# Kernel tuning notes

Measured on AMD Instinct MI355X. Metric: run time of the kernel, lower is better.

The kernel has to match this reference:

```python
import jax, jax.numpy as jnp
import numpy as np

DIM = 768
NUM_HEADS = 12
DIM_HEAD = 64
INNER = NUM_HEADS * DIM_HEAD  # 768
SCALE = DIM_HEAD ** -0.5


def setup_inputs() -> dict:
    key = jax.random.key(0)
    k1, k2, k3 = jax.random.split(key, 3)
    B, N = 8, 1024
    x = jax.random.normal(k1, (B, N, DIM), dtype=jnp.float32)
    # Linear(dim, 3*inner_dim, bias=False): weight shape (out, in) torch-style
    w_qkv = jax.random.normal(k2, (3 * INNER, DIM), dtype=jnp.float32) * (DIM ** -0.5)
    # proj: Linear(inner_dim, dim, bias=False)
    w_proj = jax.random.normal(k3, (DIM, INNER), dtype=jnp.float32) * (INNER ** -0.5)
    return {"x": x, "w_qkv": w_qkv, "w_proj": w_proj}


def reference(x, w_qkv, w_proj):
    B, N, C = x.shape
    H, dh = NUM_HEADS, DIM_HEAD
    # qkv projection: (B,N,C) @ (C, 3*inner) -> (B,N,3*inner)
    qkv = jnp.einsum('bnc,oc->bno', x, w_qkv)
    qkv = qkv.reshape(B, N, 3, H, dh).transpose(2, 0, 3, 1, 4)  # (3,B,H,N,dh)
    q, k, v = qkv[0], qkv[1], qkv[2]
    # attention scores (B,H,N,N)
    attn_scores = jnp.einsum('bhnd,bhmd->bhnm', q, k) * SCALE
    attn_probs = jax.nn.softmax(attn_scores, axis=-1)
    # attention output (B,H,N,dh) -> (B,N,inner)
    attn_out = jnp.einsum('bhnm,bhmd->bhnd', attn_probs, v)
    attn_out = attn_out.transpose(0, 2, 1, 3).reshape(B, N, H * dh)
    out = jnp.einsum('bni,oi->bno', attn_out, w_proj)
    return out
```

## Files before the change

kernel.cpp:

```cpp
#include <hip/hip_runtime.h>
#include <stdint.h>

typedef unsigned short u16;
typedef __attribute__((ext_vector_type(8))) short short8;
typedef __attribute__((ext_vector_type(4))) short short4v;
typedef __attribute__((ext_vector_type(4))) float f32x4;

#define LOG2E 1.44269504088896340736f

#define Bb 8
#define NSEQ 1024
#define DIMC 768
#define NH 12
#define DH 64
#define INNER 768
#define MTOT (Bb*NSEQ)
#define QKVN (3*INNER)
#define HEADS_TOT (Bb*NH)
#define QKV_PART ((size_t)Bb*NH*NSEQ*DH)

static __device__ inline u16 f2bf(float f) {
    uint32_t u = __builtin_bit_cast(uint32_t, f);
    uint32_t r = (u + 0x7fffu + ((u >> 16) & 1u)) >> 16;
    return (u16)r;
}

static __device__ __forceinline__ uint32_t pkbf(float f0, float f1) {
    uint32_t u0 = __builtin_bit_cast(uint32_t, f0) + 0x8000u;
    uint32_t u1 = __builtin_bit_cast(uint32_t, f1) + 0x8000u;
    return __builtin_amdgcn_perm(u1, u0, 0x07060302u);
}

#if __has_builtin(__builtin_amdgcn_mfma_f32_16x16x16bf16_1k)
static __device__ __forceinline__ f32x4 mfma16(short4v a, short4v b, f32x4 c) {
    return __builtin_amdgcn_mfma_f32_16x16x16bf16_1k(a, b, c, 0, 0, 0);
}
#else
static __device__ __forceinline__ f32x4 mfma16(short4v a, short4v b, f32x4 c) {
    asm volatile("v_mfma_f32_16x16x16_bf16 %0, %1, %2, %0\n\ts_nop 7\n\ts_nop 7"
                 : "+v"(c) : "v"(a), "v"(b));
    return c;
}
#endif

typedef __attribute__((address_space(1))) const void gas_void;
typedef __attribute__((address_space(3))) void las_void;
static __device__ __forceinline__ void async16(u16* lds, const u16* g) {
    __builtin_amdgcn_global_load_lds((gas_void*)(uintptr_t)g,
                                     (las_void*)(uintptr_t)lds, 16, 0, 0);
}

static __device__ __forceinline__ void wait_vm0() {
    __builtin_amdgcn_s_waitcnt(0x0f70);
}

#define NX8  786432
#define NWQ8 221184
#define NWP8 73728
#define NCVT (NX8 + NWQ8 + NWP8)
__global__ __launch_bounds__(256) void cvt_all(const float* __restrict__ x,
                                               const float* __restrict__ wq,
                                               const float* __restrict__ wp,
                                               u16* __restrict__ xb,
                                               u16* __restrict__ wqb,
                                               u16* __restrict__ wpb) {
    int i = blockIdx.x * 256 + threadIdx.x;
    const float* s; u16* d; int j;
    if (i < NX8) { s = x; d = xb; j = i; }
    else if (i < NX8 + NWQ8) { s = wq; d = wqb; j = i - NX8; }
    else { s = wp; d = wpb; j = i - NX8 - NWQ8; }
    const float4* s4 = (const float4*)s;
    float4 a = s4[2 * j], b = s4[2 * j + 1];
    float v[8] = {a.x, a.y, a.z, a.w, b.x, b.y, b.z, b.w};
    u16 o[8];
#pragma unroll
    for (int t = 0; t < 8; t++) o[t] = f2bf(v[t]);
    ((uint4*)d)[j] = *(const uint4*)o;
}

#define BK 32
__global__ __launch_bounds__(512, 4) void gemm_qkv(const u16* __restrict__ A,
                                                   const u16* __restrict__ Bm,
                                                   u16* __restrict__ qkv) {
    __shared__ u16 As[2][128 * BK];
    __shared__ u16 Bs[2][256 * BK];
    const int tid = threadIdx.x;
    const int w = tid >> 6, lane = tid & 63, quad = lane >> 4, l16 = lane & 15;
    const int wr = w >> 2, wc = w & 3;
    const int bid = blockIdx.x + 9 * blockIdx.y;
    const int xcd = bid & 7, j9 = bid >> 3;
    const int m0 = (8 * xcd + j9 / 9) * 128;
    const int n0 = (j9 % 9) * 256;
    const int K = DIMC;

    const int rl = lane >> 2, cc = lane & 3;
    const int ra = w * 16 + rl;
    const u16* agp = A + (size_t)(m0 + ra) * K + ((cc - ((ra >> 1) & 3)) & 3) * 8;
    const int aslot = (w * 16) * BK;
    const u16* bgp[2]; int bslot[2];
#pragma unroll
    for (int j = 0; j < 2; j++) {
        int rb = w * 32 + j * 16 + rl;
        bgp[j] = Bm + (size_t)(n0 + rb) * K + ((cc - ((rb >> 1) & 3)) & 3) * 8;
        bslot[j] = (w * 32 + j * 16) * BK;
    }

    const int swz = ((quad + ((l16 >> 1) & 3)) & 3) * 8;
    int aoff[4], boff[4];
#pragma unroll
    for (int t = 0; t < 4; t++) {
        aoff[t] = (wr * 64 + t * 16 + l16) * BK + swz;
        boff[t] = (wc * 64 + t * 16 + l16) * BK + swz;
    }

    async16(&As[0][aslot], agp);
    async16(&Bs[0][bslot[0]], bgp[0]);
    async16(&Bs[0][bslot[1]], bgp[1]);

    f32x4 acc[4][4] = {};
    const int NIT = K / BK;
    for (int it = 0; it < NIT; ++it) {
        const int cur = it & 1, nxt = cur ^ 1;
        wait_vm0();
        __syncthreads();
        if (it + 1 < NIT) {
            int ktn = (it + 1) * BK;
            async16(&As[nxt][aslot], agp + ktn);
            async16(&Bs[nxt][bslot[0]], bgp[0] + ktn);
            async16(&Bs[nxt][bslot[1]], bgp[1] + ktn);
        }
        short8 af[4], bf[4];
#pragma unroll
        for (int t = 0; t < 4; t++) af[t] = *(const short8*)(&As[cur][aoff[t]]);
#pragma unroll
        for (int t = 0; t < 4; t++) bf[t] = *(const short8*)(&Bs[cur][boff[t]]);
#pragma unroll
        for (int mt = 0; mt < 4; mt++)
#pragma unroll
            for (int nt = 0; nt < 4; nt++)
                acc[mt][nt] = __builtin_amdgcn_mfma_f32_16x16x32_bf16(af[mt], bf[nt],
                                                                      acc[mt][nt], 0, 0, 0);
    }

#pragma unroll
    for (int nt = 0; nt < 4; nt++) {
        int o = n0 + wc * 64 + nt * 16 + l16;
        int which = o / 768;
        int rem = o - which * 768;
        int h = rem >> 6, d = rem & 63;
        if (which == 2) {
            u16* vt = qkv + 2 * QKV_PART;
#pragma unroll
            for (int mt = 0; mt < 4; mt++) {
                int m = m0 + wr * 64 + mt * 16 + quad * 4;
                int bb = m >> 10, ns = m & 1023;
                alignas(8) u16 pk[4];
#pragma unroll
                for (int r = 0; r < 4; r++) pk[r] = f2bf(acc[mt][nt][r]);
                *(uint2*)(vt + ((size_t)(bb * NH + h) * DH + d) * NSEQ + ns) =
                    *(const uint2*)pk;
            }
        } else {
            float sc = (which == 0) ? (0.125f * LOG2E) : 1.0f;
#pragma unroll
            for (int mt = 0; mt < 4; mt++)
#pragma unroll
                for (int r = 0; r < 4; r++) {
                    int m = m0 + wr * 64 + mt * 16 + quad * 4 + r;
                    int bb = m >> 10, ns = m & 1023;
                    size_t idx = (size_t)which * QKV_PART +
                                 (((size_t)(bb * NH + h) * NSEQ + ns) << 6) + d;
                    qkv[idx] = f2bf(acc[mt][nt][r] * sc);
                }
        }
    }
}

__global__ __launch_bounds__(256) void gemm_proj(const u16* __restrict__ A,
                                                 const u16* __restrict__ Bm,
                                                 float* __restrict__ Co) {
    __shared__ u16 As[2][128 * BK];
    __shared__ u16 Bs[2][128 * BK];
    const int tid = threadIdx.x;
    const int w = tid >> 6, lane = tid & 63, quad = lane >> 4, l16 = lane & 15;
    const int wr = w >> 1, wc = w & 1;
    const int m0 = blockIdx.y * 128;
    const int n0 = blockIdx.x * 128;
    const int K = INNER, N = DIMC;

    const int rl = lane >> 2, cc = lane & 3;
    const u16* ag[2]; const u16* bg[2]; int sl[2];
#pragma unroll
    for (int j = 0; j < 2; j++) {
        int r = w * 32 + j * 16 + rl;
        int c = ((cc - ((r >> 1) & 3)) & 3) * 8;
        ag[j] = A + (size_t)(m0 + r) * K + c;
        bg[j] = Bm + (size_t)(n0 + r) * K + c;
        sl[j] = (w * 32 + j * 16) * BK;
    }
    const int swz = ((quad + ((l16 >> 1) & 3)) & 3) * 8;
    int aoff[4], boff[4];
#pragma unroll
    for (int t = 0; t < 4; t++) {
        aoff[t] = (wr * 64 + t * 16 + l16) * BK + swz;
        boff[t] = (wc * 64 + t * 16 + l16) * BK + swz;
    }

#pragma unroll
    for (int j = 0; j < 2; j++) {
        async16(&As[0][sl[j]], ag[j]);
        async16(&Bs[0][sl[j]], bg[j]);
    }

    f32x4 acc[4][4] = {};
    const int NIT = K / BK;
    for (int it = 0; it < NIT; ++it) {
        const int cur = it & 1, nxt = cur ^ 1;
        wait_vm0();
        __syncthreads();
        if (it + 1 < NIT) {
            int ktn = (it + 1) * BK;
#pragma unroll
            for (int j = 0; j < 2; j++) {
                async16(&As[nxt][sl[j]], ag[j] + ktn);
                async16(&Bs[nxt][sl[j]], bg[j] + ktn);
            }
        }
        short8 af[4], bf[4];
#pragma unroll
        for (int t = 0; t < 4; t++) af[t] = *(const short8*)(&As[cur][aoff[t]]);
#pragma unroll
        for (int t = 0; t < 4; t++) bf[t] = *(const short8*)(&Bs[cur][boff[t]]);
#pragma unroll
        for (int mt = 0; mt < 4; mt++)
#pragma unroll
            for (int nt = 0; nt < 4; nt++)
                acc[mt][nt] = __builtin_amdgcn_mfma_f32_16x16x32_bf16(af[mt], bf[nt],
                                                                      acc[mt][nt], 0, 0, 0);
    }
#pragma unroll
    for (int mt = 0; mt < 4; mt++)
#pragma unroll
        for (int nt = 0; nt < 4; nt++) {
            int o = n0 + wc * 64 + nt * 16 + l16;
#pragma unroll
            for (int r = 0; r < 4; r++) {
                int m = m0 + wr * 64 + mt * 16 + quad * 4 + r;
                Co[(size_t)m * N + o] = acc[mt][nt][r];
            }
        }
}

__global__ __launch_bounds__(256) void attn_kernel(const u16* __restrict__ qkv,
                                                   u16* __restrict__ attn) {
    __shared__ u16 Ks[2][64 * 64];
    __shared__ u16 Vs[2][64 * 64];

    const int tid = threadIdx.x;
    const int w = tid >> 6, lane = tid & 63, quad = lane >> 4, l16 = lane & 15;
    const int bh = blockIdx.x, qt = blockIdx.y;
    const size_t headoff = (size_t)bh * NSEQ * DH;
    const u16* Qp = qkv + headoff;
    const u16* Kp = qkv + QKV_PART + headoff;
    const u16* Vtp = qkv + 2 * QKV_PART + headoff;
    const int q0 = qt * 128 + w * 32;

    const int rl8 = lane >> 3, cc8 = lane & 7;
    const u16* kg[2]; const u16* vg[2]; int ksl[2];
#pragma unroll
    for (int j = 0; j < 2; j++) {
        int r = w * 16 + j * 8 + rl8;
        int c = ((cc8 - r) & 7) * 8;
        kg[j] = Kp + (size_t)r * DH + c;
        vg[j] = Vtp + (size_t)r * NSEQ + c;
        ksl[j] = (w * 16 + j * 8) * 64;
    }

    const int sw0 = ((quad + l16) & 7) * 8;
    const int sw1 = ((quad + 4 + l16) & 7) * 8;

    short8 qf[2][2];
#pragma unroll
    for (int mf = 0; mf < 2; mf++) {
        qf[mf][0] = *(const short8*)(Qp + (size_t)(q0 + mf * 16 + l16) * DH + quad * 8);
        qf[mf][1] = *(const short8*)(Qp + (size_t)(q0 + mf * 16 + l16) * DH + 32 + quad * 8);
    }

#pragma unroll
    for (int j = 0; j < 2; j++) {
        async16(&Ks[0][ksl[j]], kg[j]);
        async16(&Vs[0][ksl[j]], vg[j]);
    }

    f32x4 oacc[2][4] = {};
    float lsum[2] = {0.f, 0.f};

    const int NIT = NSEQ / 64;
    for (int it = 0; it < NIT; ++it) {
        const int cur = it & 1, nxt = cur ^ 1;
        wait_vm0();
        __syncthreads();
        if (it + 1 < NIT) {
            int ktn = (it + 1) * 64;
#pragma unroll
            for (int j = 0; j < 2; j++) {
                async16(&Ks[nxt][ksl[j]], kg[j] + (size_t)ktn * DH);
                async16(&Vs[nxt][ksl[j]], vg[j] + ktn);
            }
        }

        short8 kf[4][2];
#pragma unroll
        for (int nt = 0; nt < 4; nt++) {
            const u16* kr = &Ks[cur][(nt * 16 + l16) * 64];
            kf[nt][0] = *(const short8*)(kr + sw0);
            kf[nt][1] = *(const short8*)(kr + sw1);
        }
        short4v vf[4][4];
#pragma unroll
        for (int nt2 = 0; nt2 < 4; nt2++) {
            int row = nt2 * 16 + l16;
#pragma unroll
            for (int c = 0; c < 4; c++) {
                int off = row * 64 + (((c * 2 + (quad >> 1) + row) & 7) << 3) + (quad & 1) * 4;
                vf[nt2][c] = *(const short4v*)(&Vs[cur][off]);
            }
        }

#pragma unroll
        for (int mf = 0; mf < 2; mf++) {
            f32x4 st[4];
#pragma unroll
            for (int nt = 0; nt < 4; nt++) {
                f32x4 z = {};
                z = __builtin_amdgcn_mfma_f32_16x16x32_bf16(kf[nt][0], qf[mf][0], z, 0, 0, 0);
                z = __builtin_amdgcn_mfma_f32_16x16x32_bf16(kf[nt][1], qf[mf][1], z, 0, 0, 0);
                st[nt] = z;
            }
            short4v pf[4];
#pragma unroll
            for (int c = 0; c < 4; c++) {
                float p0 = __builtin_amdgcn_exp2f(st[c][0]);
                float p1 = __builtin_amdgcn_exp2f(st[c][1]);
                float p2 = __builtin_amdgcn_exp2f(st[c][2]);
                float p3 = __builtin_amdgcn_exp2f(st[c][3]);
                lsum[mf] += (p0 + p1) + (p2 + p3);
                uint2 u = {pkbf(p0, p1), pkbf(p2, p3)};
                pf[c] = __builtin_bit_cast(short4v, u);
            }
#pragma unroll
            for (int nt2 = 0; nt2 < 4; nt2++)
#pragma unroll
                for (int c = 0; c < 4; c++)
                    oacc[mf][nt2] = mfma16(vf[nt2][c], pf[c], oacc[mf][nt2]);
        }
    }

#pragma unroll
    for (int mf = 0; mf < 2; mf++) {
        float v = lsum[mf];
        v += __shfl_xor(v, 16);
        v += __shfl_xor(v, 32);
        lsum[mf] = 1.0f / v;
    }

    const int b = bh / NH, h = bh - (bh / NH) * NH;
#pragma unroll
    for (int mf = 0; mf < 2; mf++) {
        int q = q0 + mf * 16 + l16;
        float inv = lsum[mf];
#pragma unroll
        for (int nt2 = 0; nt2 < 4; nt2++) {
            uint2 u = {pkbf(oacc[mf][nt2][0] * inv, oacc[mf][nt2][1] * inv),
                       pkbf(oacc[mf][nt2][2] * inv, oacc[mf][nt2][3] * inv)};
            int d = nt2 * 16 + quad * 4;
            *(uint2*)(attn + ((size_t)(b * NSEQ + q)) * INNER + h * DH + d) = u;
        }
    }
}

extern "C" void kernel_launch(void* const* d_in, const int* in_sizes, int n_in,
                              void* d_out, int out_size, void* d_ws, size_t ws_size,
                              hipStream_t stream) {
    const float* x = (const float*)d_in[0];
    const float* w_qkv = (const float*)d_in[1];
    const float* w_proj = (const float*)d_in[2];
    float* out = (float*)d_out;

    u16* xb = (u16*)d_ws;
    u16* wqkvb = xb + 6291456;
    u16* wprojb = wqkvb + 1769472;
    u16* qkvb = wprojb + 589824;
    u16* attnb = qkvb + 18874368;

    cvt_all<<<NCVT / 256, 256, 0, stream>>>(x, w_qkv, w_proj, xb, wqkvb, wprojb);

    dim3 g1(QKVN / 256, MTOT / 128);
    gemm_qkv<<<g1, 512, 0, stream>>>(xb, wqkvb, qkvb);

    dim3 g2(HEADS_TOT, NSEQ / 128);
    attn_kernel<<<g2, 256, 0, stream>>>(qkvb, attnb);

    dim3 g3(INNER / 128, MTOT / 128);
    gemm_proj<<<g3, 256, 0, stream>>>(attnb, wprojb, out);
}
```

Baseline: 186.5 us.

## Triple-buffer LDS with counted vmcnt waits and shrink proj GEMM tile

Converts the QKV GEMM, attention and projection GEMM loops from double to triple LDS buffering with a prefetch distance of two. Each loop now waits on a partial vmcnt instead of draining all loads, so the newest stage can stay in flight while the current one is computed, and it uses a bare s_barrier. The projection GEMM tile shrinks from 128x128 to 64x128, giving more blocks to fill the CUs. The cost is more LDS per block, which may limit occupancy, and waitcnt counts that must exactly match the number of loads issued per stage.

```diff
diff --git a/kernel.cpp b/kernel.cpp
--- a/kernel.cpp
+++ b/kernel.cpp
@@ -50,8 +50,9 @@
                                      (las_void*)(uintptr_t)lds, 16, 0, 0);
 }
 
-static __device__ __forceinline__ void wait_vm0() {
-    __builtin_amdgcn_s_waitcnt(0x0f70);
+template <int N>
+static __device__ __forceinline__ void wait_vm() {
+    __builtin_amdgcn_s_waitcnt(0x0f70 | N);
 }
 
 #define NX8  786432
@@ -82,8 +83,8 @@
 __global__ __launch_bounds__(512, 4) void gemm_qkv(const u16* __restrict__ A,
                                                    const u16* __restrict__ Bm,
                                                    u16* __restrict__ qkv) {
-    __shared__ u16 As[2][128 * BK];
-    __shared__ u16 Bs[2][256 * BK];
+    __shared__ u16 As[3][128 * BK];
+    __shared__ u16 Bs[3][256 * BK];
     const int tid = threadIdx.x;
     const int w = tid >> 6, lane = tid & 63, quad = lane >> 4, l16 = lane & 15;
     const int wr = w >> 2, wc = w & 3;
@@ -113,21 +114,27 @@
         boff[t] = (wc * 64 + t * 16 + l16) * BK + swz;
     }
 
-    async16(&As[0][aslot], agp);
-    async16(&Bs[0][bslot[0]], bgp[0]);
-    async16(&Bs[0][bslot[1]], bgp[1]);
+#pragma unroll
+    for (int tt = 0; tt < 2; tt++) {
+        int kt = tt * BK;
+        async16(&As[tt][aslot], agp + kt);
+        async16(&Bs[tt][bslot[0]], bgp[0] + kt);
+        async16(&Bs[tt][bslot[1]], bgp[1] + kt);
+    }
 
     f32x4 acc[4][4] = {};
     const int NIT = K / BK;
+    int cur = 0;
     for (int it = 0; it < NIT; ++it) {
-        const int cur = it & 1, nxt = cur ^ 1;
-        wait_vm0();
-        __syncthreads();
-        if (it + 1 < NIT) {
-            int ktn = (it + 1) * BK;
-            async16(&As[nxt][aslot], agp + ktn);
-            async16(&Bs[nxt][bslot[0]], bgp[0] + ktn);
-            async16(&Bs[nxt][bslot[1]], bgp[1] + ktn);
+        if (it < NIT - 1) wait_vm<3>();
+        else              wait_vm<0>();
+        __builtin_amdgcn_s_barrier();
+        if (it < NIT - 2) {
+            int pre = cur + 2; if (pre >= 3) pre -= 3;
+            int ktn = (it + 2) * BK;
+            async16(&As[pre][aslot], agp + ktn);
+            async16(&Bs[pre][bslot[0]], bgp[0] + ktn);
+            async16(&Bs[pre][bslot[1]], bgp[1] + ktn);
         }
         short8 af[4], bf[4];
 #pragma unroll
@@ -140,6 +147,7 @@
             for (int nt = 0; nt < 4; nt++)
                 acc[mt][nt] = __builtin_amdgcn_mfma_f32_16x16x32_bf16(af[mt], bf[nt],
                                                                       acc[mt][nt], 0, 0, 0);
+        cur = (cur == 2) ? 0 : cur + 1;
     }
 
 #pragma unroll
@@ -176,76 +184,80 @@
     }
 }
 
+#define PBM 64
+#define PBN 128
 __global__ __launch_bounds__(256) void gemm_proj(const u16* __restrict__ A,
                                                  const u16* __restrict__ Bm,
                                                  float* __restrict__ Co) {
-    __shared__ u16 As[2][128 * BK];
-    __shared__ u16 Bs[2][128 * BK];
+    __shared__ u16 As[3][PBM * BK];
+    __shared__ u16 Bs[3][PBN * BK];
     const int tid = threadIdx.x;
     const int w = tid >> 6, lane = tid & 63, quad = lane >> 4, l16 = lane & 15;
     const int wr = w >> 1, wc = w & 1;
-    const int m0 = blockIdx.y * 128;
-    const int n0 = blockIdx.x * 128;
+    const int m0 = blockIdx.y * PBM;
+    const int n0 = blockIdx.x * PBN;
     const int K = INNER, N = DIMC;
 
     const int rl = lane >> 2, cc = lane & 3;
-    const u16* ag[2]; const u16* bg[2]; int sl[2];
+    const int ra = w * 16 + rl;
+    const u16* agp = A + (size_t)(m0 + ra) * K + ((cc - ((ra >> 1) & 3)) & 3) * 8;
+    const int aslot = (w * 16) * BK;
+    const u16* bgp[2]; int bslot[2];
 #pragma unroll
     for (int j = 0; j < 2; j++) {
-        int r = w * 32 + j * 16 + rl;
-        int c = ((cc - ((r >> 1) & 3)) & 3) * 8;
-        ag[j] = A + (size_t)(m0 + r) * K + c;
-        bg[j] = Bm + (size_t)(n0 + r) * K + c;
-        sl[j] = (w * 32 + j * 16) * BK;
+        int rb = j * 64 + w * 16 + rl;
+        bgp[j] = Bm + (size_t)(n0 + rb) * K + ((cc - ((rb >> 1) & 3)) & 3) * 8;
+        bslot[j] = (j * 64 + w * 16) * BK;
     }
     const int swz = ((quad + ((l16 >> 1) & 3)) & 3) * 8;
-    int aoff[4], boff[4];
-#pragma unroll
-    for (int t = 0; t < 4; t++) {
-        aoff[t] = (wr * 64 + t * 16 + l16) * BK + swz;
-        boff[t] = (wc * 64 + t * 16 + l16) * BK + swz;
-    }
-
-#pragma unroll
-    for (int j = 0; j < 2; j++) {
-        async16(&As[0][sl[j]], ag[j]);
-        async16(&Bs[0][sl[j]], bg[j]);
-    }
-
-    f32x4 acc[4][4] = {};
+    int aoff[2], boff[4];
+#pragma unroll
+    for (int t = 0; t < 2; t++) aoff[t] = (wr * 32 + t * 16 + l16) * BK + swz;
+#pragma unroll
+    for (int t = 0; t < 4; t++) boff[t] = (wc * 64 + t * 16 + l16) * BK + swz;
+
+#pragma unroll
+    for (int tt = 0; tt < 2; tt++) {
+        int kt = tt * BK;
+        async16(&As[tt][aslot], agp + kt);
+        async16(&Bs[tt][bslot[0]], bgp[0] + kt);
+        async16(&Bs[tt][bslot[1]], bgp[1] + kt);
+    }
+
+    f32x4 acc[2][4] = {};
     const int NIT = K / BK;
+    int cur = 0;
     for (int it = 0; it < NIT; ++it) {
-        const int cur = it & 1, nxt = cur ^ 1;
-        wait_vm0();
-        __syncthreads();
-        if (it + 1 < NIT) {
-            int ktn = (it + 1) * BK;
-#pragma unroll
-            for (int j = 0; j < 2; j++) {
-                async16(&As[nxt][sl[j]], ag[j] + ktn);
-                async16(&Bs[nxt][sl[j]], bg[j] + ktn);
-            }
-        }
-        short8 af[4], bf[4];
-#pragma unroll
-        for (int t = 0; t < 4; t++) af[t] = *(const short8*)(&As[cur][aoff[t]]);
+        if (it < NIT - 1) wait_vm<3>(); else wait_vm<0>();
+        __builtin_amdgcn_s_barrier();
+        if (it < NIT - 2) {
+            int pre = cur + 2; if (pre >= 3) pre -= 3;
+            int ktn = (it + 2) * BK;
+            async16(&As[pre][aslot], agp + ktn);
+            async16(&Bs[pre][bslot[0]], bgp[0] + ktn);
+            async16(&Bs[pre][bslot[1]], bgp[1] + ktn);
+        }
+        short8 af[2], bf[4];
+#pragma unroll
+        for (int t = 0; t < 2; t++) af[t] = *(const short8*)(&As[cur][aoff[t]]);
 #pragma unroll
         for (int t = 0; t < 4; t++) bf[t] = *(const short8*)(&Bs[cur][boff[t]]);
 #pragma unroll
-        for (int mt = 0; mt < 4; mt++)
+        for (int mt = 0; mt < 2; mt++)
 #pragma unroll
             for (int nt = 0; nt < 4; nt++)
                 acc[mt][nt] = __builtin_amdgcn_mfma_f32_16x16x32_bf16(af[mt], bf[nt],
                                                                       acc[mt][nt], 0, 0, 0);
-    }
-#pragma unroll
-    for (int mt = 0; mt < 4; mt++)
+        cur = (cur == 2) ? 0 : cur + 1;
+    }
+#pragma unroll
+    for (int mt = 0; mt < 2; mt++)
 #pragma unroll
         for (int nt = 0; nt < 4; nt++) {
             int o = n0 + wc * 64 + nt * 16 + l16;
 #pragma unroll
             for (int r = 0; r < 4; r++) {
-                int m = m0 + wr * 64 + mt * 16 + quad * 4 + r;
+                int m = m0 + wr * 32 + mt * 16 + quad * 4 + r;
                 Co[(size_t)m * N + o] = acc[mt][nt][r];
             }
         }
@@ -253,8 +265,8 @@
 
 __global__ __launch_bounds__(256) void attn_kernel(const u16* __restrict__ qkv,
                                                    u16* __restrict__ attn) {
-    __shared__ u16 Ks[2][64 * 64];
-    __shared__ u16 Vs[2][64 * 64];
+    __shared__ u16 Ks[3][64 * 64];
+    __shared__ u16 Vs[3][64 * 64];
 
     const int tid = threadIdx.x;
     const int w = tid >> 6, lane = tid & 63, quad = lane >> 4, l16 = lane & 15;
@@ -287,25 +299,33 @@
     }
 
 #pragma unroll
-    for (int j = 0; j < 2; j++) {
-        async16(&Ks[0][ksl[j]], kg[j]);
-        async16(&Vs[0][ksl[j]], vg[j]);
-    }
+    for (int tt = 0; tt < 3; tt++) {
+        int kt = tt * 64;
+#pragma unroll
+        for (int j = 0; j < 2; j++) {
+            async16(&Ks[tt][ksl[j]], kg[j] + (size_t)kt * DH);
+            async16(&Vs[tt][ksl[j]], vg[j] + kt);
+        }
+    }
+    asm volatile("" :: "v"(qf[0][0]), "v"(qf[0][1]), "v"(qf[1][0]), "v"(qf[1][1]));
 
     f32x4 oacc[2][4] = {};
     float lsum[2] = {0.f, 0.f};
 
     const int NIT = NSEQ / 64;
+    int cur = 0;
     for (int it = 0; it < NIT; ++it) {
-        const int cur = it & 1, nxt = cur ^ 1;
-        wait_vm0();
-        __syncthreads();
-        if (it + 1 < NIT) {
-            int ktn = (it + 1) * 64;
+        if (it == 0)          wait_vm<8>();
+        else if (it < NIT - 1) wait_vm<4>();
+        else                   wait_vm<0>();
+        __builtin_amdgcn_s_barrier();
+        if (it >= 1 && it < NIT - 2) {
+            int pre = cur + 2; if (pre >= 3) pre -= 3;
+            int ktn = (it + 2) * 64;
 #pragma unroll
             for (int j = 0; j < 2; j++) {
-                async16(&Ks[nxt][ksl[j]], kg[j] + (size_t)ktn * DH);
-                async16(&Vs[nxt][ksl[j]], vg[j] + ktn);
+                async16(&Ks[pre][ksl[j]], kg[j] + (size_t)ktn * DH);
+                async16(&Vs[pre][ksl[j]], vg[j] + ktn);
             }
         }
 
@@ -354,6 +374,7 @@
                 for (int c = 0; c < 4; c++)
                     oacc[mf][nt2] = mfma16(vf[nt2][c], pf[c], oacc[mf][nt2]);
         }
+        cur = (cur == 2) ? 0 : cur + 1;
     }
 
 #pragma unroll
@@ -401,6 +422,6 @@
     dim3 g2(HEADS_TOT, NSEQ / 128);
     attn_kernel<<<g2, 256, 0, stream>>>(qkvb, attnb);
 
-    dim3 g3(INNER / 128, MTOT / 128);
+    dim3 g3(INNER / PBN, MTOT / PBM);
     gemm_proj<<<g3, 256, 0, stream>>>(attnb, wprojb, out);
 }
```

Result: no change. 185.9 us (-0.3%).
